# Performance work log

Hardware: AMD Instinct MI355X
Metric: run time of the kernel (lower is better)

Reference implementation:

```python
import jax, jax.numpy as jnp
import numpy as np
import math

B, S, H = 2, 2048, 1024
NH, HD = 16, 64  # num heads, head dim; NH*HD == H


def setup_inputs() -> dict:
    key = jax.random.key(0)
    k1, k2, k3 = jax.random.split(key, 3)
    hidden_states = jax.random.normal(k1, (B, S, H), dtype=jnp.float32)
    # causal multiplicative mask [1,1,S,S], 1.0 where attending is allowed
    mask = jnp.tril(jnp.ones((S, S), dtype=jnp.float32))[None, None]
    W_qkv = jax.random.normal(k2, (H, 3 * H), dtype=jnp.float32) * (1.0 / math.sqrt(H))
    b_qkv = jnp.zeros((3 * H,), dtype=jnp.float32)
    W_out = jax.random.normal(k3, (H, H), dtype=jnp.float32) * (1.0 / math.sqrt(H))
    b_out = jnp.zeros((H,), dtype=jnp.float32)
    return {"hidden_states": hidden_states, "mask": mask, "W_qkv": W_qkv,
            "b_qkv": b_qkv, "W_out": W_out, "b_out": b_out}


def reference(hidden_states, mask, W_qkv, b_qkv, W_out, b_out):
    b, s, h = hidden_states.shape
    # fused QKV projection then split into contiguous thirds (split_tensor_along_last_dim)
    qkv = jnp.einsum('bsh,hd->bsd', hidden_states, W_qkv) + b_qkv
    q, k, v = jnp.split(qkv, 3, axis=-1)
    # [b, s, nh*hd] -> [b, nh, s, hd]
    def to_heads(t):
        return t.reshape(b, s, NH, HD).transpose(0, 2, 1, 3)
    q, k, v = to_heads(q), to_heads(k), to_heads(v)
    q = q / jnp.sqrt(jnp.float32(HD))  # scaling_attention_score=True
    scores = jnp.einsum('bhqd,bhkd->bhqk', q, k)  # [b,nh,s,s]
    # multiplicative mask + large-negative bias trick from standard_attention
    scores = scores * mask - 10000.0 * (1.0 - mask)
    probs = jax.nn.softmax(scores, axis=-1)
    ctx = jnp.einsum('bhqk,bhkd->bhqd', probs, v)
    ctx = ctx.transpose(0, 2, 1, 3).reshape(b, s, h)  # [b, s, nh*hd]
    return jnp.einsum('bsh,hd->bsd', ctx, W_out) + b_out
```

## Files before the change

### kernel.cpp

```cpp
#include <hip/hip_runtime.h>
#include <cstdint>
#include <cstddef>

#define NHEAD 16
#define HDIM 64
#define SEQ 2048
#define BATCH 2
#define HID 1024

typedef __bf16 bf16x8 __attribute__((ext_vector_type(8)));
typedef __bf16 bf16x2_t __attribute__((ext_vector_type(2)));
typedef float f32x4 __attribute__((ext_vector_type(4)));

__device__ __forceinline__ unsigned short f2bf(float f) {
    union { float f; unsigned u; } v; v.f = f;
    unsigned r = v.u + 0x7fffu + ((v.u >> 16) & 1u);
    return (unsigned short)(r >> 16);
}

__device__ __forceinline__ unsigned pk_bf16(float a, float b) {
#if __has_builtin(__builtin_amdgcn_cvt_pk_bf16_f32)
    bf16x2_t p = __builtin_amdgcn_cvt_pk_bf16_f32(a, b);
    return __builtin_bit_cast(unsigned, p);
#else
    return (unsigned)f2bf(a) | ((unsigned)f2bf(b) << 16);
#endif
}

__device__ __forceinline__ void transpose_tile(
    const float* __restrict__ in, unsigned short* __restrict__ out,
    int R, int C, int bx, int by, int t) {
    __shared__ unsigned short T[64][72];
    int c0 = bx * 64, r0 = by * 64;
    for (int p = 0; p < 4; ++p) {
        int idx = (p * 256 + t) * 4;
        int row = idx >> 6, col = idx & 63;
        float4 v = *(const float4*)(in + (size_t)(r0 + row) * C + c0 + col);
        T[row][col + 0] = f2bf(v.x);
        T[row][col + 1] = f2bf(v.y);
        T[row][col + 2] = f2bf(v.z);
        T[row][col + 3] = f2bf(v.w);
    }
    __syncthreads();
    for (int p = 0; p < 4; ++p) {
        int idx = (p * 256 + t) * 4;
        int orow = idx >> 6, ocol = idx & 63;
        ushort4 u;
        u.x = T[ocol + 0][orow];
        u.y = T[ocol + 1][orow];
        u.z = T[ocol + 2][orow];
        u.w = T[ocol + 3][orow];
        *(ushort4*)(out + (size_t)(c0 + orow) * R + r0 + ocol) = u;
    }
}

__global__ __launch_bounds__(256) void prep(
    const float* __restrict__ X, unsigned short* __restrict__ Xb,
    const float* __restrict__ W1, unsigned short* __restrict__ W1t,
    const float* __restrict__ W2, unsigned short* __restrict__ W2t) {
    int blk = blockIdx.x, t = threadIdx.x;
    if (blk < 2048) {
        int i = (blk * 256 + t) * 8;
        float4 a = *(const float4*)(X + i);
        float4 b = *(const float4*)(X + i + 4);
        uint4 o;
        o.x = pk_bf16(a.x, a.y);
        o.y = pk_bf16(a.z, a.w);
        o.z = pk_bf16(b.x, b.y);
        o.w = pk_bf16(b.z, b.w);
        *(uint4*)(Xb + i) = o;
    } else if (blk < 2816) {
        int r = blk - 2048;
        transpose_tile(W1, W1t, 1024, 3072, r % 48, r / 48, t);
    } else {
        int r = blk - 2816;
        transpose_tile(W2, W2t, 1024, 1024, r % 16, r / 16, t);
    }
}

__global__ __launch_bounds__(256) void transpose_v(
    const unsigned short* __restrict__ in, unsigned short* __restrict__ out) {
    __shared__ unsigned short T[64][72];
    int t = threadIdx.x;
    int s0 = blockIdx.x * 64, bh = blockIdx.y;
    const unsigned short* ip = in + (size_t)bh * SEQ * HDIM;
    unsigned short* op = out + (size_t)bh * HDIM * SEQ;
    for (int p = 0; p < 2; ++p) {
        int idx = (p * 256 + t) * 8;
        int row = idx >> 6, col = idx & 63;
        *(uint4*)&T[row][col] = *(const uint4*)(ip + (size_t)(s0 + row) * HDIM + col);
    }
    __syncthreads();
    for (int p = 0; p < 4; ++p) {
        int idx = (p * 256 + t) * 4;
        int d = idx >> 6, c = idx & 63;
        ushort4 u;
        u.x = T[c + 0][d];
        u.y = T[c + 1][d];
        u.z = T[c + 2][d];
        u.w = T[c + 3][d];
        *(ushort4*)(op + (size_t)d * SEQ + s0 + c) = u;
    }
}

#define GEMM_DB_BODY(Aptr, Btptr, KDIM)                                                  \
    __shared__ unsigned short As[2][128][32];                                            \
    __shared__ unsigned short Bs[2][128][32];                                            \
    int t = threadIdx.x;                                                                 \
    int wave = t >> 6, lane = t & 63, ln = lane & 15, quad = lane >> 4;                  \
    int wm = wave >> 1, wn = wave & 1;                                                   \
    int m0 = blockIdx.y * 128, n0 = blockIdx.x * 128;                                    \
    int srow = lane >> 2, scol = (lane & 3) * 8;                                         \
    f32x4 zero4 = {0.f, 0.f, 0.f, 0.f};                                                  \
    f32x4 acc[4][4];                                                                     \
    for (int mi = 0; mi < 4; ++mi)                                                       \
        for (int ni = 0; ni < 4; ++ni) acc[mi][ni] = zero4;                              \
    auto stage = [&](int kt, int bi) {                                                   \
        for (int p = 0; p < 2; ++p) {                                                    \
            int r0 = (wave * 2 + p) * 16 + srow;                                         \
            __builtin_amdgcn_global_load_lds(                                            \
                (const __attribute__((address_space(1))) void*)                          \
                    ((Aptr) + (size_t)(m0 + r0) * (KDIM) + kt + scol),                   \
                (__attribute__((address_space(3))) void*)&As[bi][(wave * 2 + p) * 16][0],\
                16, 0, 0);                                                               \
            __builtin_amdgcn_global_load_lds(                                            \
                (const __attribute__((address_space(1))) void*)                          \
                    ((Btptr) + (size_t)(n0 + r0) * (KDIM) + kt + scol),                  \
                (__attribute__((address_space(3))) void*)&Bs[bi][(wave * 2 + p) * 16][0],\
                16, 0, 0);                                                               \
        }                                                                                \
    };                                                                                   \
    stage(0, 0);                                                                         \
    const int NIT = (KDIM) / 32;                                                         \
    for (int it = 0; it < NIT; ++it) {                                                   \
        __syncthreads();                                                                 \
        if (it + 1 < NIT) stage((it + 1) * 32, (it + 1) & 1);                            \
        int bi = it & 1;                                                                 \
        bf16x8 af[4], bfr[4];                                                            \
        for (int mi = 0; mi < 4; ++mi)                                                   \
            af[mi] = *(const bf16x8*)&As[bi][wm * 64 + mi * 16 + ln][quad * 8];          \
        for (int ni = 0; ni < 4; ++ni)                                                   \
            bfr[ni] = *(const bf16x8*)&Bs[bi][wn * 64 + ni * 16 + ln][quad * 8];         \
        for (int mi = 0; mi < 4; ++mi)                                                   \
            for (int ni = 0; ni < 4; ++ni)                                               \
                acc[mi][ni] = __builtin_amdgcn_mfma_f32_16x16x32_bf16(                   \
                    af[mi], bfr[ni], acc[mi][ni], 0, 0, 0);                              \
    }

__global__ __launch_bounds__(256) void gemm_qkv(
    const unsigned short* __restrict__ A, const unsigned short* __restrict__ Bt,
    const float* __restrict__ bias,
    unsigned short* __restrict__ Qb, unsigned short* __restrict__ Kb,
    unsigned short* __restrict__ Vtmp) {
    GEMM_DB_BODY(A, Bt, 1024)
    int nbase = n0 + wn * 64;
    for (int ni = 0; ni < 4; ++ni) {
        int gn = nbase + ni * 16 + ln;
        float bv = bias[gn];
        int third = gn >> 10;
        int rem = gn & 1023;
        int h = rem >> 6, d = rem & 63;
        unsigned short* dst = third == 0 ? Qb : (third == 1 ? Kb : Vtmp);
        float scale = third == 0 ? 0.1803368801111f : 1.0f;
        for (int mi = 0; mi < 4; ++mi) {
            for (int r = 0; r < 4; ++r) {
                int gm = m0 + wm * 64 + mi * 16 + quad * 4 + r;
                int b = gm >> 11, s = gm & 2047;
                size_t bh = (size_t)(b * NHEAD + h);
                dst[(bh * SEQ + s) * HDIM + d] = f2bf((acc[mi][ni][r] + bv) * scale);
            }
        }
    }
}

__global__ __launch_bounds__(256) void gemm_out(
    const unsigned short* __restrict__ A, const unsigned short* __restrict__ Bt,
    const float* __restrict__ bias, float* __restrict__ C) {
    __shared__ unsigned short As[2][64][32];
    __shared__ unsigned short Bs[2][128][32];
    int t = threadIdx.x;
    int wave = t >> 6, lane = t & 63, ln = lane & 15, quad = lane >> 4;
    int wm = wave >> 1, wn = wave & 1;
    int m0 = blockIdx.y * 64, n0 = blockIdx.x * 128;
    int srow = lane >> 2, scol = (lane & 3) * 8;
    f32x4 zero4 = {0.f, 0.f, 0.f, 0.f};
    f32x4 acc[2][4];
    for (int mi = 0; mi < 2; ++mi)
        for (int ni = 0; ni < 4; ++ni) acc[mi][ni] = zero4;
    auto stage = [&](int kt, int bi) {
        for (int c = wave * 3; c < wave * 3 + 3; ++c) {
            if (c < 4) {
                __builtin_amdgcn_global_load_lds(
                    (const __attribute__((address_space(1))) void*)
                        (A + (size_t)(m0 + c * 16 + srow) * 1024 + kt + scol),
                    (__attribute__((address_space(3))) void*)&As[bi][c * 16][0], 16, 0, 0);
            } else {
                int cb = c - 4;
                __builtin_amdgcn_global_load_lds(
                    (const __attribute__((address_space(1))) void*)
                        (Bt + (size_t)(n0 + cb * 16 + srow) * 1024 + kt + scol),
                    (__attribute__((address_space(3))) void*)&Bs[bi][cb * 16][0], 16, 0, 0);
            }
        }
    };
    stage(0, 0);
    for (int it = 0; it < 32; ++it) {
        __syncthreads();
        if (it + 1 < 32) stage((it + 1) * 32, (it + 1) & 1);
        int bi = it & 1;
        bf16x8 af[2], bfr[4];
        for (int mi = 0; mi < 2; ++mi)
            af[mi] = *(const bf16x8*)&As[bi][wm * 32 + mi * 16 + ln][quad * 8];
        for (int ni = 0; ni < 4; ++ni)
            bfr[ni] = *(const bf16x8*)&Bs[bi][wn * 64 + ni * 16 + ln][quad * 8];
        for (int mi = 0; mi < 2; ++mi)
            for (int ni = 0; ni < 4; ++ni)
                acc[mi][ni] = __builtin_amdgcn_mfma_f32_16x16x32_bf16(
                    af[mi], bfr[ni], acc[mi][ni], 0, 0, 0);
    }
    for (int ni = 0; ni < 4; ++ni) {
        int gn = n0 + wn * 64 + ni * 16 + ln;
        float bv = bias[gn];
        for (int mi = 0; mi < 2; ++mi) {
            for (int r = 0; r < 4; ++r) {
                int gm = m0 + wm * 32 + mi * 16 + quad * 4 + r;
                C[(size_t)gm * HID + gn] = acc[mi][ni][r] + bv;
            }
        }
    }
}

__global__ __launch_bounds__(256) void flash_attn(
    const unsigned short* __restrict__ Qb, const unsigned short* __restrict__ Kb,
    const unsigned short* __restrict__ Vt, unsigned short* __restrict__ Ctx) {
    __shared__ unsigned short KsB[2][64][64];
    __shared__ unsigned short VsB[2][64][64];
    __shared__ unsigned short Ps[4][16][72];
    int tid = threadIdx.x;
    int wave = tid >> 6, lane = tid & 63, ln = lane & 15, quad = lane >> 4;
    int bh = blockIdx.y;
    int qiA = (bh < 16) ? blockIdx.x : (15 - blockIdx.x);
    int qiB = 31 - qiA;
    int q0A = qiA * 64, q0B = qiB * 64;
    const size_t baseQK = (size_t)bh * SEQ * HDIM;
    const size_t baseV = (size_t)bh * HDIM * SEQ;
    int b = bh >> 4, h = bh & 15;

    int rIn = lane >> 3;
    int gsw = ((lane & 7) ^ rIn) * 8;

    bf16x8 aqA0, aqA1, aqB0, aqB1;
    {
        const unsigned short* qp =
            Qb + baseQK + (size_t)(q0A + wave * 16 + ln) * HDIM + quad * 8;
        aqA0 = *(const bf16x8*)qp;
        aqA1 = *(const bf16x8*)(qp + 32);
        qp = Qb + baseQK + (size_t)(q0B + wave * 16 + ln) * HDIM + quad * 8;
        aqB0 = *(const bf16x8*)qp;
        aqB1 = *(const bf16x8*)(qp + 32);
    }

    auto prefetch = [&](int kj, int bi) {
        const unsigned short* kb = Kb + baseQK + (size_t)kj * 64 * HDIM;
        const unsigned short* vb = Vt + baseV + kj * 64;
        for (int c = wave; c < 8; c += 4) {
            __builtin_amdgcn_global_load_lds(
                (const __attribute__((address_space(1))) void*)(kb + (c * 8 + rIn) * HDIM + gsw),
                (__attribute__((address_space(3))) void*)&KsB[bi][c * 8][0], 16, 0, 0);
            __builtin_amdgcn_global_load_lds(
                (const __attribute__((address_space(1))) void*)(vb + (size_t)(c * 8 + rIn) * SEQ + gsw),
                (__attribute__((address_space(3))) void*)&VsB[bi][c * 8][0], 16, 0, 0);
        }
    };

    f32x4 zero4 = {0.f, 0.f, 0.f, 0.f};
    f32x4 oA[4], oB[4];
    float laccA = 0.f, laccB = 0.f;
    for (int i = 0; i < 4; ++i) { oA[i] = zero4; oB[i] = zero4; }

    auto epilogue = [&](f32x4* o, float lacc, int q0) {
        float sum = lacc;
        sum += __shfl_xor(sum, 16);
        sum += __shfl_xor(sum, 32);
        float linv = __builtin_amdgcn_rcpf(sum);
        size_t rowb = ((size_t)(b * SEQ + q0 + wave * 16 + ln)) * HID + h * 64;
        for (int ni = 0; ni < 4; ++ni) {
            uint2 u;
            u.x = pk_bf16(o[ni][0] * linv, o[ni][1] * linv);
            u.y = pk_bf16(o[ni][2] * linv, o[ni][3] * linv);
            *(uint2*)&Ctx[rowb + ni * 16 + quad * 4] = u;
        }
    };

    prefetch(0, 0);
    for (int k = 0; k <= qiB; ++k) {
        __syncthreads();
        if (k < qiB) prefetch(k + 1, (k + 1) & 1);
        int buf = k & 1;

        {
            f32x4 s4[4];
            for (int ni = 0; ni < 4; ++ni) s4[ni] = zero4;
            for (int kk = 0; kk < 2; ++kk) {
                bf16x8 bq = kk ? aqB1 : aqB0;
                for (int ni = 0; ni < 4; ++ni) {
                    bf16x8 ak = *(const bf16x8*)
                        &KsB[buf][ni * 16 + ln][((kk * 4 + quad) ^ (ln & 7)) * 8];
                    s4[ni] = __builtin_amdgcn_mfma_f32_16x16x32_bf16(ak, bq, s4[ni], 0, 0, 0);
                }
            }
            if (k == qiB) {
                for (int ni = 0; ni < 4; ++ni)
                    for (int r = 0; r < 4; ++r)
                        if (ni * 16 + quad * 4 + r > wave * 16 + ln) s4[ni][r] = -1.0e38f;
            }
            for (int ni = 0; ni < 4; ++ni) {
                float e0 = __builtin_amdgcn_exp2f(s4[ni][0]);
                float e1 = __builtin_amdgcn_exp2f(s4[ni][1]);
                float e2 = __builtin_amdgcn_exp2f(s4[ni][2]);
                float e3 = __builtin_amdgcn_exp2f(s4[ni][3]);
                laccB += (e0 + e1) + (e2 + e3);
                uint2 pk;
                pk.x = pk_bf16(e0, e1);
                pk.y = pk_bf16(e2, e3);
                *(uint2*)&Ps[wave][ln][ni * 16 + quad * 4] = pk;
            }
            for (int kk = 0; kk < 2; ++kk) {
                bf16x8 bp = *(const bf16x8*)&Ps[wave][ln][kk * 32 + quad * 8];
                for (int ni = 0; ni < 4; ++ni) {
                    bf16x8 av = *(const bf16x8*)
                        &VsB[buf][ni * 16 + ln][((kk * 4 + quad) ^ (ln & 7)) * 8];
                    oB[ni] = __builtin_amdgcn_mfma_f32_16x16x32_bf16(av, bp, oB[ni], 0, 0, 0);
                }
            }
        }

        if (k <= qiA) {
            f32x4 s4[4];
            for (int ni = 0; ni < 4; ++ni) s4[ni] = zero4;
            for (int kk = 0; kk < 2; ++kk) {
                bf16x8 bq = kk ? aqA1 : aqA0;
                for (int ni = 0; ni < 4; ++ni) {
                    bf16x8 ak = *(const bf16x8*)
                        &KsB[buf][ni * 16 + ln][((kk * 4 + quad) ^ (ln & 7)) * 8];
                    s4[ni] = __builtin_amdgcn_mfma_f32_16x16x32_bf16(ak, bq, s4[ni], 0, 0, 0);
                }
            }
            if (k == qiA) {
                for (int ni = 0; ni < 4; ++ni)
                    for (int r = 0; r < 4; ++r)
                        if (ni * 16 + quad * 4 + r > wave * 16 + ln) s4[ni][r] = -1.0e38f;
            }
            for (int ni = 0; ni < 4; ++ni) {
                float e0 = __builtin_amdgcn_exp2f(s4[ni][0]);
                float e1 = __builtin_amdgcn_exp2f(s4[ni][1]);
                float e2 = __builtin_amdgcn_exp2f(s4[ni][2]);
                float e3 = __builtin_amdgcn_exp2f(s4[ni][3]);
                laccA += (e0 + e1) + (e2 + e3);
                uint2 pk;
                pk.x = pk_bf16(e0, e1);
                pk.y = pk_bf16(e2, e3);
                *(uint2*)&Ps[wave][ln][ni * 16 + quad * 4] = pk;
            }
            for (int kk = 0; kk < 2; ++kk) {
                bf16x8 bp = *(const bf16x8*)&Ps[wave][ln][kk * 32 + quad * 8];
                for (int ni = 0; ni < 4; ++ni) {
                    bf16x8 av = *(const bf16x8*)
                        &VsB[buf][ni * 16 + ln][((kk * 4 + quad) ^ (ln & 7)) * 8];
                    oA[ni] = __builtin_amdgcn_mfma_f32_16x16x32_bf16(av, bp, oA[ni], 0, 0, 0);
                }
            }
            if (k == qiA) epilogue(oA, laccA, q0A);
        }
    }
    epilogue(oB, laccB, q0B);
}

extern "C" void kernel_launch(void* const* d_in, const int* in_sizes, int n_in,
                              void* d_out, int out_size, void* d_ws, size_t ws_size,
                              hipStream_t stream) {
    const float* X = (const float*)d_in[0];
    const float* Wqkv = (const float*)d_in[2];
    const float* bqkv = (const float*)d_in[3];
    const float* Wout = (const float*)d_in[4];
    const float* bout = (const float*)d_in[5];
    float* out = (float*)d_out;

    char* ws = (char*)d_ws;
    unsigned short* Xb   = (unsigned short*)(ws + 0);
    unsigned short* Vt   = (unsigned short*)(ws + 0);
    unsigned short* W1t  = (unsigned short*)(ws + 8388608);
    unsigned short* W2t  = (unsigned short*)(ws + 14680064);
    unsigned short* Qb   = (unsigned short*)(ws + 16777216);
    unsigned short* Kb   = (unsigned short*)(ws + 25165824);
    unsigned short* Vtmp = (unsigned short*)(ws + 33554432);
    unsigned short* Ctx  = (unsigned short*)(ws + 41943040);

    prep<<<3072, 256, 0, stream>>>(X, Xb, Wqkv, W1t, Wout, W2t);
    gemm_qkv<<<dim3(24, 32), 256, 0, stream>>>(Xb, W1t, bqkv, Qb, Kb, Vtmp);
    transpose_v<<<dim3(32, 32), 256, 0, stream>>>(Vtmp, Vt);
    flash_attn<<<dim3(16, 32), 256, 0, stream>>>(Qb, Kb, Vt, Ctx);
    gemm_out<<<dim3(8, 64), 256, 0, stream>>>(Ctx, W2t, bout, out);
}
```

Measured before the change: 208.9 us.

## Split paired causal query tiles into one tile per block, drop K/V double buffering

Each block now handles a single 64-row query tile instead of a balanced pair of tiles (i and 31-i). The grid doubles to 1024 blocks, and tiles are assigned with a rotation by batch-head index. K/V staging goes from a double-buffered prefetch to a single buffer loaded synchronously each iteration with two barriers, which halves the LDS footprint. This gains parallelism and occupancy, but gives up the load balance of the pairing, the reuse of each K/V tile across two query tiles, and the overlap of loads with compute.

```diff
diff --git a/kernel.cpp b/kernel.cpp
--- a/kernel.cpp
+++ b/kernel.cpp
@@ -233,15 +233,14 @@
 __global__ __launch_bounds__(256) void flash_attn(
     const unsigned short* __restrict__ Qb, const unsigned short* __restrict__ Kb,
     const unsigned short* __restrict__ Vt, unsigned short* __restrict__ Ctx) {
-    __shared__ unsigned short KsB[2][64][64];
-    __shared__ unsigned short VsB[2][64][64];
+    __shared__ unsigned short Ks[64][64];
+    __shared__ unsigned short Vs[64][64];
     __shared__ unsigned short Ps[4][16][72];
     int tid = threadIdx.x;
     int wave = tid >> 6, lane = tid & 63, ln = lane & 15, quad = lane >> 4;
     int bh = blockIdx.y;
-    int qiA = (bh < 16) ? blockIdx.x : (15 - blockIdx.x);
-    int qiB = 31 - qiA;
-    int q0A = qiA * 64, q0B = qiB * 64;
+    int qi = (blockIdx.x + bh) & 31;
+    int q0 = qi * 64;
     const size_t baseQK = (size_t)bh * SEQ * HDIM;
     const size_t baseV = (size_t)bh * HDIM * SEQ;
     int b = bh >> 4, h = bh & 15;
@@ -249,131 +248,80 @@
     int rIn = lane >> 3;
     int gsw = ((lane & 7) ^ rIn) * 8;
 
-    bf16x8 aqA0, aqA1, aqB0, aqB1;
+    bf16x8 aq0, aq1;
     {
         const unsigned short* qp =
-            Qb + baseQK + (size_t)(q0A + wave * 16 + ln) * HDIM + quad * 8;
-        aqA0 = *(const bf16x8*)qp;
-        aqA1 = *(const bf16x8*)(qp + 32);
-        qp = Qb + baseQK + (size_t)(q0B + wave * 16 + ln) * HDIM + quad * 8;
-        aqB0 = *(const bf16x8*)qp;
-        aqB1 = *(const bf16x8*)(qp + 32);
-    }
-
-    auto prefetch = [&](int kj, int bi) {
-        const unsigned short* kb = Kb + baseQK + (size_t)kj * 64 * HDIM;
-        const unsigned short* vb = Vt + baseV + kj * 64;
-        for (int c = wave; c < 8; c += 4) {
-            __builtin_amdgcn_global_load_lds(
-                (const __attribute__((address_space(1))) void*)(kb + (c * 8 + rIn) * HDIM + gsw),
-                (__attribute__((address_space(3))) void*)&KsB[bi][c * 8][0], 16, 0, 0);
-            __builtin_amdgcn_global_load_lds(
-                (const __attribute__((address_space(1))) void*)(vb + (size_t)(c * 8 + rIn) * SEQ + gsw),
-                (__attribute__((address_space(3))) void*)&VsB[bi][c * 8][0], 16, 0, 0);
-        }
-    };
+            Qb + baseQK + (size_t)(q0 + wave * 16 + ln) * HDIM + quad * 8;
+        aq0 = *(const bf16x8*)qp;
+        aq1 = *(const bf16x8*)(qp + 32);
+    }
 
     f32x4 zero4 = {0.f, 0.f, 0.f, 0.f};
-    f32x4 oA[4], oB[4];
-    float laccA = 0.f, laccB = 0.f;
-    for (int i = 0; i < 4; ++i) { oA[i] = zero4; oB[i] = zero4; }
-
-    auto epilogue = [&](f32x4* o, float lacc, int q0) {
-        float sum = lacc;
-        sum += __shfl_xor(sum, 16);
-        sum += __shfl_xor(sum, 32);
-        float linv = __builtin_amdgcn_rcpf(sum);
-        size_t rowb = ((size_t)(b * SEQ + q0 + wave * 16 + ln)) * HID + h * 64;
+    f32x4 o[4];
+    float lacc = 0.f;
+    for (int i = 0; i < 4; ++i) o[i] = zero4;
+
+    for (int k = 0; k <= qi; ++k) {
+        {
+            const unsigned short* kb = Kb + baseQK + (size_t)k * 64 * HDIM;
+            const unsigned short* vb = Vt + baseV + k * 64;
+            for (int c = wave; c < 8; c += 4) {
+                __builtin_amdgcn_global_load_lds(
+                    (const __attribute__((address_space(1))) void*)(kb + (c * 8 + rIn) * HDIM + gsw),
+                    (__attribute__((address_space(3))) void*)&Ks[c * 8][0], 16, 0, 0);
+                __builtin_amdgcn_global_load_lds(
+                    (const __attribute__((address_space(1))) void*)(vb + (size_t)(c * 8 + rIn) * SEQ + gsw),
+                    (__attribute__((address_space(3))) void*)&Vs[c * 8][0], 16, 0, 0);
+            }
+        }
+        __syncthreads();
+
+        f32x4 s4[4];
         for (int ni = 0; ni < 4; ++ni) {
-            uint2 u;
-            u.x = pk_bf16(o[ni][0] * linv, o[ni][1] * linv);
-            u.y = pk_bf16(o[ni][2] * linv, o[ni][3] * linv);
-            *(uint2*)&Ctx[rowb + ni * 16 + quad * 4] = u;
-        }
-    };
-
-    prefetch(0, 0);
-    for (int k = 0; k <= qiB; ++k) {
-        __syncthreads();
-        if (k < qiB) prefetch(k + 1, (k + 1) & 1);
-        int buf = k & 1;
-
-        {
-            f32x4 s4[4];
-            for (int ni = 0; ni < 4; ++ni) s4[ni] = zero4;
-            for (int kk = 0; kk < 2; ++kk) {
-                bf16x8 bq = kk ? aqB1 : aqB0;
-                for (int ni = 0; ni < 4; ++ni) {
-                    bf16x8 ak = *(const bf16x8*)
-                        &KsB[buf][ni * 16 + ln][((kk * 4 + quad) ^ (ln & 7)) * 8];
-                    s4[ni] = __builtin_amdgcn_mfma_f32_16x16x32_bf16(ak, bq, s4[ni], 0, 0, 0);
-                }
-            }
-            if (k == qiB) {
-                for (int ni = 0; ni < 4; ++ni)
-                    for (int r = 0; r < 4; ++r)
-                        if (ni * 16 + quad * 4 + r > wave * 16 + ln) s4[ni][r] = -1.0e38f;
-            }
+            bf16x8 ak0 = *(const bf16x8*)&Ks[ni * 16 + ln][(quad ^ (ln & 7)) * 8];
+            bf16x8 ak1 = *(const bf16x8*)&Ks[ni * 16 + ln][((4 + quad) ^ (ln & 7)) * 8];
+            s4[ni] = __builtin_amdgcn_mfma_f32_16x16x32_bf16(ak0, aq0, zero4, 0, 0, 0);
+            s4[ni] = __builtin_amdgcn_mfma_f32_16x16x32_bf16(ak1, aq1, s4[ni], 0, 0, 0);
+        }
+        if (k == qi) {
+            for (int ni = 0; ni < 4; ++ni)
+                for (int r = 0; r < 4; ++r)
+                    if (ni * 16 + quad * 4 + r > wave * 16 + ln) s4[ni][r] = -1.0e38f;
+        }
+
+        for (int ni = 0; ni < 4; ++ni) {
+            float e0 = __builtin_amdgcn_exp2f(s4[ni][0]);
+            float e1 = __builtin_amdgcn_exp2f(s4[ni][1]);
+            float e2 = __builtin_amdgcn_exp2f(s4[ni][2]);
+            float e3 = __builtin_amdgcn_exp2f(s4[ni][3]);
+            lacc += (e0 + e1) + (e2 + e3);
+            uint2 pk;
+            pk.x = pk_bf16(e0, e1);
+            pk.y = pk_bf16(e2, e3);
+            *(uint2*)&Ps[wave][ln][ni * 16 + quad * 4] = pk;
+        }
+        for (int kk = 0; kk < 2; ++kk) {
+            bf16x8 bp = *(const bf16x8*)&Ps[wave][ln][kk * 32 + quad * 8];
             for (int ni = 0; ni < 4; ++ni) {
-                float e0 = __builtin_amdgcn_exp2f(s4[ni][0]);
-                float e1 = __builtin_amdgcn_exp2f(s4[ni][1]);
-                float e2 = __builtin_amdgcn_exp2f(s4[ni][2]);
-                float e3 = __builtin_amdgcn_exp2f(s4[ni][3]);
-                laccB += (e0 + e1) + (e2 + e3);
-                uint2 pk;
-                pk.x = pk_bf16(e0, e1);
-                pk.y = pk_bf16(e2, e3);
-                *(uint2*)&Ps[wave][ln][ni * 16 + quad * 4] = pk;
-            }
-            for (int kk = 0; kk < 2; ++kk) {
-                bf16x8 bp = *(const bf16x8*)&Ps[wave][ln][kk * 32 + quad * 8];
-                for (int ni = 0; ni < 4; ++ni) {
-                    bf16x8 av = *(const bf16x8*)
-                        &VsB[buf][ni * 16 + ln][((kk * 4 + quad) ^ (ln & 7)) * 8];
-                    oB[ni] = __builtin_amdgcn_mfma_f32_16x16x32_bf16(av, bp, oB[ni], 0, 0, 0);
-                }
-            }
-        }
-
-        if (k <= qiA) {
-            f32x4 s4[4];
-            for (int ni = 0; ni < 4; ++ni) s4[ni] = zero4;
-            for (int kk = 0; kk < 2; ++kk) {
-                bf16x8 bq = kk ? aqA1 : aqA0;
-                for (int ni = 0; ni < 4; ++ni) {
-                    bf16x8 ak = *(const bf16x8*)
-                        &KsB[buf][ni * 16 + ln][((kk * 4 + quad) ^ (ln & 7)) * 8];
-                    s4[ni] = __builtin_amdgcn_mfma_f32_16x16x32_bf16(ak, bq, s4[ni], 0, 0, 0);
-                }
-            }
-            if (k == qiA) {
-                for (int ni = 0; ni < 4; ++ni)
-                    for (int r = 0; r < 4; ++r)
-                        if (ni * 16 + quad * 4 + r > wave * 16 + ln) s4[ni][r] = -1.0e38f;
-            }
-            for (int ni = 0; ni < 4; ++ni) {
-                float e0 = __builtin_amdgcn_exp2f(s4[ni][0]);
-                float e1 = __builtin_amdgcn_exp2f(s4[ni][1]);
-                float e2 = __builtin_amdgcn_exp2f(s4[ni][2]);
-                float e3 = __builtin_amdgcn_exp2f(s4[ni][3]);
-                laccA += (e0 + e1) + (e2 + e3);
-                uint2 pk;
-                pk.x = pk_bf16(e0, e1);
-                pk.y = pk_bf16(e2, e3);
-                *(uint2*)&Ps[wave][ln][ni * 16 + quad * 4] = pk;
-            }
-            for (int kk = 0; kk < 2; ++kk) {
-                bf16x8 bp = *(const bf16x8*)&Ps[wave][ln][kk * 32 + quad * 8];
-                for (int ni = 0; ni < 4; ++ni) {
-                    bf16x8 av = *(const bf16x8*)
-                        &VsB[buf][ni * 16 + ln][((kk * 4 + quad) ^ (ln & 7)) * 8];
-                    oA[ni] = __builtin_amdgcn_mfma_f32_16x16x32_bf16(av, bp, oA[ni], 0, 0, 0);
-                }
-            }
-            if (k == qiA) epilogue(oA, laccA, q0A);
-        }
-    }
-    epilogue(oB, laccB, q0B);
+                bf16x8 av = *(const bf16x8*)
+                    &Vs[ni * 16 + ln][((kk * 4 + quad) ^ (ln & 7)) * 8];
+                o[ni] = __builtin_amdgcn_mfma_f32_16x16x32_bf16(av, bp, o[ni], 0, 0, 0);
+            }
+        }
+        if (k < qi) __syncthreads();
+    }
+
+    float sum = lacc;
+    sum += __shfl_xor(sum, 16);
+    sum += __shfl_xor(sum, 32);
+    float linv = __builtin_amdgcn_rcpf(sum);
+    size_t rowb = ((size_t)(b * SEQ + q0 + wave * 16 + ln)) * HID + h * 64;
+    for (int ni = 0; ni < 4; ++ni) {
+        uint2 u;
+        u.x = pk_bf16(o[ni][0] * linv, o[ni][1] * linv);
+        u.y = pk_bf16(o[ni][2] * linv, o[ni][3] * linv);
+        *(uint2*)&Ctx[rowb + ni * 16 + quad * 4] = u;
+    }
 }
 
 extern "C" void kernel_launch(void* const* d_in, const int* in_sizes, int n_in,
@@ -399,6 +347,6 @@
     prep<<<3072, 256, 0, stream>>>(X, Xb, Wqkv, W1t, Wout, W2t);
     gemm_qkv<<<dim3(24, 32), 256, 0, stream>>>(Xb, W1t, bqkv, Qb, Kb, Vtmp);
     transpose_v<<<dim3(32, 32), 256, 0, stream>>>(Vtmp, Vt);
-    flash_attn<<<dim3(16, 32), 256, 0, stream>>>(Qb, Kb, Vt, Ctx);
+    flash_attn<<<dim3(32, 32), 256, 0, stream>>>(Qb, Kb, Vt, Ctx);
     gemm_out<<<dim3(8, 64), 256, 0, stream>>>(Ctx, W2t, bout, out);
 }
```

Measured after the change: 215.4 us. 1.03x slower.
